# Performance work log

Measured on AMD Instinct MI355X. Metric: run time of the kernel, lower is better.

## Reference

```python
import jax, jax.numpy as jnp
import numpy as np

B, H, S, D = 4, 16, 2048, 64

def setup_inputs() -> dict:
    key = jax.random.key(0)
    kq, kk, kv = jax.random.split(key, 3)
    query = jax.random.normal(kq, (B, H, S, D), dtype=jnp.float32)
    key_t = jax.random.normal(kk, (B, H, S, D), dtype=jnp.float32)
    value = jax.random.normal(kv, (B, H, S, D), dtype=jnp.float32)
    return {"query": query, "key": key_t, "value": value}

def reference(query, key, value):
    d = query.shape[-1]
    scale = 1.0 / jnp.sqrt(jnp.asarray(d, dtype=query.dtype))
    # scores: [B, H, S_q, S_k]
    scores = jnp.einsum('bhqd,bhkd->bhqk', query, key) * scale
    p_attn = jax.nn.softmax(scores, axis=-1)
    # out: [B, H, S_q, D]
    return jnp.einsum('bhqk,bhkd->bhqd', p_attn, value)
```

## Files before the change

kernel.cpp:

```cpp
#include <hip/hip_runtime.h>
#include <hip/hip_bf16.h>


constexpr int Sdim = 2048;
constexpr int Ddim = 64;
constexpr int QBLK = 128;
constexpr int KVBLK = 64;
constexpr int NBH = 64;
constexpr int NT = Sdim / KVBLK;
constexpr int TILE_E = KVBLK * Ddim;
constexpr float QSCALE = 0.125f * 1.44269504f;
constexpr float DEFER_THR = 11.0f;

typedef __attribute__((ext_vector_type(8))) short short8;
typedef __attribute__((ext_vector_type(4))) float f32x4;
typedef __attribute__((ext_vector_type(4))) unsigned short ushort4v;
typedef __attribute__((ext_vector_type(2))) unsigned int uint2v;

typedef __attribute__((address_space(1))) const unsigned int GU32;
typedef __attribute__((address_space(3))) unsigned int LU32;

__device__ __forceinline__ unsigned short f2bf(float f) {
    union { float f; unsigned int u; } v; v.f = f;
    unsigned int r = v.u + 0x7FFFu + ((v.u >> 16) & 1u);
    return (unsigned short)(r >> 16);
}

__device__ __forceinline__ unsigned int cvt_pk_bf16(float lo, float hi) {
    unsigned int r;
    asm("v_cvt_pk_bf16_f32 %0, %1, %2" : "=v"(r) : "v"(lo), "v"(hi));
    return r;
}

__device__ __forceinline__ void gload_lds16(const unsigned short* g, unsigned short* l) {
    __builtin_amdgcn_global_load_lds((GU32*)g, (LU32*)l, 16, 0, 0);
}

__global__ __launch_bounds__(256)
void prep_k(const float* __restrict__ Kg, unsigned short* __restrict__ Kbf) {
    size_t idx = ((size_t)blockIdx.x * 256 + threadIdx.x) * 4;
    int c0 = (int)(idx & 63);
    size_t row = idx >> 6;
    int swz = ((int)row & 7) << 3;
    float4 f = *(const float4*)(Kg + idx);
    ushort4v h;
    h.x = f2bf(f.x); h.y = f2bf(f.y); h.z = f2bf(f.z); h.w = f2bf(f.w);
    *(ushort4v*)(Kbf + (row << 6) + (c0 ^ swz)) = h;
}

__global__ __launch_bounds__(256)
void prep_v(const float* __restrict__ Vg, unsigned short* __restrict__ Vtb) {
    __shared__ unsigned short Vl[KVBLK][Ddim + 4];
    int bh = blockIdx.x >> 5, t = blockIdx.x & 31;
    const float* src = Vg + ((size_t)bh * Sdim + t * KVBLK) * Ddim;
    unsigned short* dst = Vtb + ((size_t)bh * NT + t) * TILE_E;

    {
        int kv = threadIdx.x >> 2;
        int dq = (threadIdx.x & 3) * 16;
#pragma unroll
        for (int i = 0; i < 4; ++i) {
            float4 f = *(const float4*)(src + (size_t)kv * Ddim + dq + 4 * i);
            ushort4v h;
            h.x = f2bf(f.x); h.y = f2bf(f.y); h.z = f2bf(f.z); h.w = f2bf(f.w);
            *(ushort4v*)&Vl[kv][dq + 4 * i] = h;
        }
    }
    __syncthreads();
    {
        int d  = threadIdx.x >> 2;
        int sc = (threadIdx.x & 3) * 16;
        int swzd = (d & 7) << 3;
#pragma unroll
        for (int u = 0; u < 4; ++u) {
            int s0 = sc + 4 * u;
            int kc = s0 >> 5, g = (s0 >> 3) & 3, h = (s0 >> 2) & 1;
            int kvb = 32 * kc + 16 * h + 4 * g;
            ushort4v o;
            o.x = Vl[kvb + 0][d]; o.y = Vl[kvb + 1][d];
            o.z = Vl[kvb + 2][d]; o.w = Vl[kvb + 3][d];
            *(ushort4v*)(dst + (size_t)d * KVBLK + (s0 ^ swzd)) = o;
        }
    }
}

__global__ __launch_bounds__(512, 4)
void attn_fwd_fast(const float* __restrict__ Qg, const unsigned short* __restrict__ Kbf,
                   const unsigned short* __restrict__ Vtb, float* __restrict__ Og)
{
    __shared__ unsigned short Kt[2][KVBLK][Ddim];
    __shared__ unsigned short Vt[2][Ddim][KVBLK];

    const int tid = threadIdx.x;
    const int w   = tid >> 6;
    const int l   = tid & 63;
    const int g   = l >> 4;
    const int q   = l & 15;
    const int swz = (q & 7) << 3;

    const int bh = blockIdx.y;
    const size_t base = (size_t)bh * Sdim * Ddim;
    const int q0 = blockIdx.x * QBLK;

    const unsigned short* kbase = Kbf + base;
    const unsigned short* vbase = Vtb + base;
    const int eo = tid * 8;

    short8 qf[2];
    {
        const float* qrow = Qg + base + (size_t)(q0 + w * 16 + q) * Ddim;
#pragma unroll
        for (int kc = 0; kc < 2; ++kc) {
            float fv[8];
            *(float4*)(fv)     = *(const float4*)(qrow + kc * 32 + g * 8);
            *(float4*)(fv + 4) = *(const float4*)(qrow + kc * 32 + g * 8 + 4);
            short8 r;
#pragma unroll
            for (int j = 0; j < 8; ++j) r[j] = (short)f2bf(fv[j] * QSCALE);
            qf[kc] = r;
        }
    }

    f32x4 o[4];
#pragma unroll
    for (int dt = 0; dt < 4; ++dt)
#pragma unroll
        for (int r = 0; r < 4; ++r) o[dt][r] = 0.0f;
    float m_run = 0.0f;
    float l_part = 0.0f;

    union PU { unsigned int u[4]; short8 s8; };

    gload_lds16(kbase + eo, &Kt[0][0][0] + w * 512);
    gload_lds16(vbase + eo, &Vt[0][0][0] + w * 512);

    for (int t = 0; t < NT; ++t) {
        const int cur = t & 1;
        if (t + 1 < NT) {
            const unsigned short* kn = kbase + (size_t)(t + 1) * TILE_E;
            const unsigned short* vn = vbase + (size_t)(t + 1) * TILE_E;
            gload_lds16(kn + eo, &Kt[cur ^ 1][0][0] + w * 512);
            gload_lds16(vn + eo, &Vt[cur ^ 1][0][0] + w * 512);
            asm volatile("s_waitcnt vmcnt(2)" ::: "memory");
        } else {
            asm volatile("s_waitcnt vmcnt(0)" ::: "memory");
        }
        __builtin_amdgcn_s_barrier();
        __builtin_amdgcn_sched_barrier(0);

        f32x4 sa[4];
#pragma unroll
        for (int nt = 0; nt < 4; ++nt)
#pragma unroll
            for (int r = 0; r < 4; ++r) sa[nt][r] = -m_run;
        __builtin_amdgcn_s_setprio(1);
#pragma unroll
        for (int kc = 0; kc < 2; ++kc)
#pragma unroll
            for (int nt = 0; nt < 4; ++nt) {
                const short8 kf = *(const short8*)&Kt[cur][nt * 16 + q][(kc * 32 + g * 8) ^ swz];
                sa[nt] = __builtin_amdgcn_mfma_f32_16x16x32_bf16(kf, qf[kc], sa[nt], 0, 0, 0);
            }
        __builtin_amdgcn_s_setprio(0);

        f32x4 m4 = sa[0];
#pragma unroll
        for (int nt = 1; nt < 4; ++nt)
#pragma unroll
            for (int r = 0; r < 4; ++r) m4[r] = fmaxf(m4[r], sa[nt][r]);
        float mx = fmaxf(fmaxf(m4[0], m4[1]), fmaxf(m4[2], m4[3]));
        mx = fmaxf(mx, __shfl_xor(mx, 16));
        mx = fmaxf(mx, __shfl_xor(mx, 32));

        PU pa[2];
        float ts = 0.0f;
        if (__all(mx <= DEFER_THR)) {
#pragma unroll
            for (int nt = 0; nt < 4; ++nt) {
                float e0 = exp2f(sa[nt][0]), e1 = exp2f(sa[nt][1]);
                float e2 = exp2f(sa[nt][2]), e3 = exp2f(sa[nt][3]);
                ts += (e0 + e1) + (e2 + e3);
                pa[nt >> 1].u[(nt & 1) * 2 + 0] = cvt_pk_bf16(e0, e1);
                pa[nt >> 1].u[(nt & 1) * 2 + 1] = cvt_pk_bf16(e2, e3);
            }
            l_part += ts;
        } else {
            float fr = exp2f(-mx);
            m_run += mx;
#pragma unroll
            for (int nt = 0; nt < 4; ++nt) {
                float e0 = exp2f(sa[nt][0] - mx), e1 = exp2f(sa[nt][1] - mx);
                float e2 = exp2f(sa[nt][2] - mx), e3 = exp2f(sa[nt][3] - mx);
                ts += (e0 + e1) + (e2 + e3);
                pa[nt >> 1].u[(nt & 1) * 2 + 0] = cvt_pk_bf16(e0, e1);
                pa[nt >> 1].u[(nt & 1) * 2 + 1] = cvt_pk_bf16(e2, e3);
            }
            l_part = l_part * fr + ts;
            float frb[4];
#pragma unroll
            for (int r = 0; r < 4; ++r) frb[r] = __shfl(fr, 4 * g + r);
#pragma unroll
            for (int dt = 0; dt < 4; ++dt)
#pragma unroll
                for (int r = 0; r < 4; ++r) o[dt][r] *= frb[r];
        }

        __builtin_amdgcn_s_setprio(1);
#pragma unroll
        for (int kc = 0; kc < 2; ++kc)
#pragma unroll
            for (int dt = 0; dt < 4; ++dt) {
                const short8 vf = *(const short8*)&Vt[cur][dt * 16 + q][(kc * 32 + g * 8) ^ swz];
                o[dt] = __builtin_amdgcn_mfma_f32_16x16x32_bf16(pa[kc].s8, vf, o[dt], 0, 0, 0);
            }
        __builtin_amdgcn_s_setprio(0);

        if (t + 1 < NT) {
            __builtin_amdgcn_sched_barrier(0);
            __builtin_amdgcn_s_barrier();
        }
    }

    l_part += __shfl_xor(l_part, 16);
    l_part += __shfl_xor(l_part, 32);
    float inv = 1.0f / l_part;
    float invb[4];
#pragma unroll
    for (int r = 0; r < 4; ++r) invb[r] = __shfl(inv, 4 * g + r);
#pragma unroll
    for (int r = 0; r < 4; ++r) {
        float* orow = Og + base + (size_t)(q0 + w * 16 + 4 * g + r) * Ddim;
#pragma unroll
        for (int dt = 0; dt < 4; ++dt) orow[dt * 16 + q] = o[dt][r] * invb[r];
    }
}

__global__ __launch_bounds__(256, 4)
void attn_fwd_slow(const float* __restrict__ Qg, const float* __restrict__ Kg,
                   const float* __restrict__ Vg, float* __restrict__ Og)
{
    __shared__ unsigned short Kt[KVBLK][Ddim];
    __shared__ unsigned short Vt[Ddim][KVBLK];
    __shared__ unsigned short Pt[4][16][KVBLK];

    const int tid = threadIdx.x;
    const int w   = tid >> 6;
    const int l   = tid & 63;
    const int g   = l >> 4;
    const int q   = l & 15;
    const int swz = (q & 7) << 3;

    const size_t base = (size_t)blockIdx.y * Sdim * Ddim;
    const int q0 = blockIdx.x * 64;

    short8 qf[2];
    {
        const float* qrow = Qg + base + (size_t)(q0 + w * 16 + q) * Ddim;
#pragma unroll
        for (int kc = 0; kc < 2; ++kc) {
            float fv[8];
            *(float4*)(fv)     = *(const float4*)(qrow + kc * 32 + g * 8);
            *(float4*)(fv + 4) = *(const float4*)(qrow + kc * 32 + g * 8 + 4);
            short8 r;
#pragma unroll
            for (int j = 0; j < 8; ++j) r[j] = (short)f2bf(fv[j] * QSCALE);
            qf[kc] = r;
        }
    }

    f32x4 o[4];
#pragma unroll
    for (int dt = 0; dt < 4; ++dt)
#pragma unroll
        for (int r = 0; r < 4; ++r) o[dt][r] = 0.0f;
    float m_run = -INFINITY, l_run = 0.0f;

    for (int t = 0; t < NT; ++t) {
        __syncthreads();
        {
            const float* Ksrc = Kg + base + (size_t)t * KVBLK * Ddim;
            const float* Vsrc = Vg + base + (size_t)t * KVBLK * Ddim;
#pragma unroll
            for (int it = 0; it < 4; ++it) {
                int idx = it * 1024 + tid * 4;
                int r = idx >> 6, c = idx & 63;
                float4 kf4 = *(const float4*)(Ksrc + idx);
                ushort4v hk;
                hk.x = f2bf(kf4.x); hk.y = f2bf(kf4.y);
                hk.z = f2bf(kf4.z); hk.w = f2bf(kf4.w);
                *(ushort4v*)&Kt[r][c ^ ((r & 7) << 3)] = hk;
            }
            {
                const int d = l;
                const int vswz = (d & 7) << 3;
#pragma unroll
                for (int i = 0; i < 4; ++i) {
                    int kv0 = w * 16 + i * 4;
                    float a0 = Vsrc[(size_t)(kv0 + 0) * Ddim + d];
                    float a1 = Vsrc[(size_t)(kv0 + 1) * Ddim + d];
                    float a2 = Vsrc[(size_t)(kv0 + 2) * Ddim + d];
                    float a3 = Vsrc[(size_t)(kv0 + 3) * Ddim + d];
                    ushort4v hv;
                    hv.x = f2bf(a0); hv.y = f2bf(a1);
                    hv.z = f2bf(a2); hv.w = f2bf(a3);
                    *(ushort4v*)&Vt[d][kv0 ^ vswz] = hv;
                }
            }
        }
        __syncthreads();

        f32x4 sa[4];
#pragma unroll
        for (int nt = 0; nt < 4; ++nt)
#pragma unroll
            for (int r = 0; r < 4; ++r) sa[nt][r] = 0.0f;
#pragma unroll
        for (int kc = 0; kc < 2; ++kc)
#pragma unroll
            for (int nt = 0; nt < 4; ++nt) {
                const short8 kf = *(const short8*)&Kt[nt * 16 + q][(kc * 32 + g * 8) ^ swz];
                sa[nt] = __builtin_amdgcn_mfma_f32_16x16x32_bf16(kf, qf[kc], sa[nt], 0, 0, 0);
            }

        float mx = sa[0][0];
#pragma unroll
        for (int nt = 0; nt < 4; ++nt)
#pragma unroll
            for (int r = 0; r < 4; ++r) mx = fmaxf(mx, sa[nt][r]);
        mx = fmaxf(mx, __shfl_xor(mx, 16));
        mx = fmaxf(mx, __shfl_xor(mx, 32));
        float mnew = fmaxf(m_run, mx);
        float fr = exp2f(m_run - mnew);
        m_run = mnew;

        float p[4][4];
        float s = 0.0f;
#pragma unroll
        for (int nt = 0; nt < 4; ++nt)
#pragma unroll
            for (int r = 0; r < 4; ++r) {
                float e = exp2f(sa[nt][r] - mnew);
                p[nt][r] = e; s += e;
            }
        s += __shfl_xor(s, 16);
        s += __shfl_xor(s, 32);
        l_run = l_run * fr + s;

#pragma unroll
        for (int nt = 0; nt < 4; ++nt) {
            uint2v pp;
            pp.x = cvt_pk_bf16(p[nt][0], p[nt][1]);
            pp.y = cvt_pk_bf16(p[nt][2], p[nt][3]);
            *(uint2v*)&Pt[w][q][(nt * 16 + 4 * g) ^ swz] = pp;
        }

        float frb[4];
#pragma unroll
        for (int r = 0; r < 4; ++r) frb[r] = __shfl(fr, 4 * g + r);
#pragma unroll
        for (int dt = 0; dt < 4; ++dt)
#pragma unroll
            for (int r = 0; r < 4; ++r) o[dt][r] *= frb[r];

#pragma unroll
        for (int kc = 0; kc < 2; ++kc) {
            const short8 pf = *(const short8*)&Pt[w][q][(kc * 32 + g * 8) ^ swz];
#pragma unroll
            for (int dt = 0; dt < 4; ++dt) {
                const short8 vf = *(const short8*)&Vt[dt * 16 + q][(kc * 32 + g * 8) ^ swz];
                o[dt] = __builtin_amdgcn_mfma_f32_16x16x32_bf16(pf, vf, o[dt], 0, 0, 0);
            }
        }
    }

    float inv = 1.0f / l_run;
    float invb[4];
#pragma unroll
    for (int r = 0; r < 4; ++r) invb[r] = __shfl(inv, 4 * g + r);
#pragma unroll
    for (int r = 0; r < 4; ++r) {
        float* orow = Og + base + (size_t)(q0 + w * 16 + 4 * g + r) * Ddim;
#pragma unroll
        for (int dt = 0; dt < 4; ++dt) orow[dt * 16 + q] = o[dt][r] * invb[r];
    }
}

extern "C" void kernel_launch(void* const* d_in, const int* in_sizes, int n_in,
                              void* d_out, int out_size, void* d_ws, size_t ws_size,
                              hipStream_t stream) {
    const float* Q = (const float*)d_in[0];
    const float* K = (const float*)d_in[1];
    const float* V = (const float*)d_in[2];
    float* O = (float*)d_out;
    const size_t elems = (size_t)NBH * Sdim * Ddim;
    const size_t need  = elems * 2 * 2;
    if (ws_size >= need) {
        unsigned short* Kbf = (unsigned short*)d_ws;
        unsigned short* Vtb = Kbf + elems;
        prep_k<<<dim3((unsigned)(elems / 4 / 256)), dim3(256), 0, stream>>>(K, Kbf);
        prep_v<<<dim3(NBH * NT), dim3(256), 0, stream>>>(V, Vtb);
        attn_fwd_fast<<<dim3(Sdim / QBLK, NBH), dim3(512), 0, stream>>>(Q, Kbf, Vtb, O);
    } else {
        attn_fwd_slow<<<dim3(Sdim / 64, NBH), dim3(256), 0, stream>>>(Q, K, V, O);
    }
}
```

Measured before the change: 249.5 us.

## Give each wave two query sub-tiles to reuse K/V fragments; merge prep kernels

The attention kernel now runs 4 waves of 256 threads instead of 8, and each wave handles 32 query rows as two 16-row groups. Every K and V fragment read from LDS now feeds two MFMAs, which halves LDS read traffic per FLOP and doubles the loads each thread issues per tile. The K and V bf16 prep kernels are merged into a single launch to save one kernel launch. In exchange, register use per thread roughly doubles for accumulators and scores, and there are fewer waves per workgroup to hide latency.

New measurement: 424.4 us. +70.1%, slower.

```diff
diff --git a/kernel.cpp b/kernel.cpp
--- a/kernel.cpp
+++ b/kernel.cpp
@@ -15,6 +15,7 @@
 typedef __attribute__((ext_vector_type(8))) short short8;
 typedef __attribute__((ext_vector_type(4))) float f32x4;
 typedef __attribute__((ext_vector_type(4))) unsigned short ushort4v;
+typedef __attribute__((ext_vector_type(4))) unsigned int uint4v;
 typedef __attribute__((ext_vector_type(2))) unsigned int uint2v;
 
 typedef __attribute__((address_space(1))) const unsigned int GU32;
@@ -36,25 +37,28 @@
     __builtin_amdgcn_global_load_lds((GU32*)g, (LU32*)l, 16, 0, 0);
 }
 
+constexpr int KPB = (NBH * Sdim * Ddim) / 4 / 256;
+constexpr int VPB = NBH * NT;
+
 __global__ __launch_bounds__(256)
-void prep_k(const float* __restrict__ Kg, unsigned short* __restrict__ Kbf) {
-    size_t idx = ((size_t)blockIdx.x * 256 + threadIdx.x) * 4;
-    int c0 = (int)(idx & 63);
-    size_t row = idx >> 6;
-    int swz = ((int)row & 7) << 3;
-    float4 f = *(const float4*)(Kg + idx);
-    ushort4v h;
-    h.x = f2bf(f.x); h.y = f2bf(f.y); h.z = f2bf(f.z); h.w = f2bf(f.w);
-    *(ushort4v*)(Kbf + (row << 6) + (c0 ^ swz)) = h;
-}
-
-__global__ __launch_bounds__(256)
-void prep_v(const float* __restrict__ Vg, unsigned short* __restrict__ Vtb) {
+void prep_kv(const float* __restrict__ Kg, const float* __restrict__ Vg,
+             unsigned short* __restrict__ Kbf, unsigned short* __restrict__ Vtb) {
     __shared__ unsigned short Vl[KVBLK][Ddim + 4];
-    int bh = blockIdx.x >> 5, t = blockIdx.x & 31;
+    if (blockIdx.x < KPB) {
+        size_t idx = ((size_t)blockIdx.x * 256 + threadIdx.x) * 4;
+        int c0 = (int)(idx & 63);
+        size_t row = idx >> 6;
+        int swz = ((int)row & 7) << 3;
+        float4 f = *(const float4*)(Kg + idx);
+        ushort4v h;
+        h.x = f2bf(f.x); h.y = f2bf(f.y); h.z = f2bf(f.z); h.w = f2bf(f.w);
+        *(ushort4v*)(Kbf + (row << 6) + (c0 ^ swz)) = h;
+        return;
+    }
+    int bid = blockIdx.x - KPB;
+    int bh = bid >> 5, t = bid & 31;
     const float* src = Vg + ((size_t)bh * Sdim + t * KVBLK) * Ddim;
     unsigned short* dst = Vtb + ((size_t)bh * NT + t) * TILE_E;
-
     {
         int kv = threadIdx.x >> 2;
         int dq = (threadIdx.x & 3) * 16;
@@ -84,12 +88,12 @@
     }
 }
 
-__global__ __launch_bounds__(512, 4)
+__global__ __launch_bounds__(256, 4)
 void attn_fwd_fast(const float* __restrict__ Qg, const unsigned short* __restrict__ Kbf,
                    const unsigned short* __restrict__ Vtb, float* __restrict__ Og)
 {
-    __shared__ unsigned short Kt[2][KVBLK][Ddim];
-    __shared__ unsigned short Vt[2][Ddim][KVBLK];
+    __shared__ unsigned short Kt[2][TILE_E];
+    __shared__ unsigned short Vt[2][TILE_E];
 
     const int tid = threadIdx.x;
     const int w   = tid >> 6;
@@ -105,10 +109,12 @@
     const unsigned short* kbase = Kbf + base;
     const unsigned short* vbase = Vtb + base;
     const int eo = tid * 8;
-
-    short8 qf[2];
-    {
-        const float* qrow = Qg + base + (size_t)(q0 + w * 16 + q) * Ddim;
+    const int stoff = w * 512;
+
+    short8 qf[2][2];
+#pragma unroll
+    for (int gg = 0; gg < 2; ++gg) {
+        const float* qrow = Qg + base + (size_t)(q0 + w * 32 + gg * 16 + q) * Ddim;
 #pragma unroll
         for (int kc = 0; kc < 2; ++kc) {
             float fv[8];
@@ -117,102 +123,130 @@
             short8 r;
 #pragma unroll
             for (int j = 0; j < 8; ++j) r[j] = (short)f2bf(fv[j] * QSCALE);
-            qf[kc] = r;
-        }
-    }
-
-    f32x4 o[4];
-#pragma unroll
-    for (int dt = 0; dt < 4; ++dt)
-#pragma unroll
-        for (int r = 0; r < 4; ++r) o[dt][r] = 0.0f;
-    float m_run = 0.0f;
-    float l_part = 0.0f;
-
-    union PU { unsigned int u[4]; short8 s8; };
-
-    gload_lds16(kbase + eo, &Kt[0][0][0] + w * 512);
-    gload_lds16(vbase + eo, &Vt[0][0][0] + w * 512);
+            qf[gg][kc] = r;
+        }
+    }
+
+    f32x4 o_[2][4];
+#pragma unroll
+    for (int gg = 0; gg < 2; ++gg)
+#pragma unroll
+        for (int dt = 0; dt < 4; ++dt)
+#pragma unroll
+            for (int r = 0; r < 4; ++r) o_[gg][dt][r] = 0.0f;
+    float m_run[2] = {0.0f, 0.0f};
+    float l_part[2] = {0.0f, 0.0f};
+
+    gload_lds16(kbase + eo,        &Kt[0][0] + stoff);
+    gload_lds16(kbase + 2048 + eo, &Kt[0][0] + 2048 + stoff);
+    gload_lds16(vbase + eo,        &Vt[0][0] + stoff);
+    gload_lds16(vbase + 2048 + eo, &Vt[0][0] + 2048 + stoff);
 
     for (int t = 0; t < NT; ++t) {
         const int cur = t & 1;
         if (t + 1 < NT) {
-            const unsigned short* kn = kbase + (size_t)(t + 1) * TILE_E;
-            const unsigned short* vn = vbase + (size_t)(t + 1) * TILE_E;
-            gload_lds16(kn + eo, &Kt[cur ^ 1][0][0] + w * 512);
-            gload_lds16(vn + eo, &Vt[cur ^ 1][0][0] + w * 512);
-            asm volatile("s_waitcnt vmcnt(2)" ::: "memory");
+            const size_t toff = (size_t)(t + 1) * TILE_E + eo;
+            unsigned short* kd = &Kt[cur ^ 1][0];
+            unsigned short* vd = &Vt[cur ^ 1][0];
+            gload_lds16(kbase + toff,        kd + stoff);
+            gload_lds16(kbase + toff + 2048, kd + 2048 + stoff);
+            gload_lds16(vbase + toff,        vd + stoff);
+            gload_lds16(vbase + toff + 2048, vd + 2048 + stoff);
+            asm volatile("s_waitcnt vmcnt(4)" ::: "memory");
         } else {
             asm volatile("s_waitcnt vmcnt(0)" ::: "memory");
         }
         __builtin_amdgcn_s_barrier();
         __builtin_amdgcn_sched_barrier(0);
 
-        f32x4 sa[4];
-#pragma unroll
-        for (int nt = 0; nt < 4; ++nt)
-#pragma unroll
-            for (int r = 0; r < 4; ++r) sa[nt][r] = -m_run;
+        const unsigned short* kb = &Kt[cur][0];
+        const unsigned short* vb = &Vt[cur][0];
+
+        f32x4 sa[2][4];
+#pragma unroll
+        for (int gg = 0; gg < 2; ++gg)
+#pragma unroll
+            for (int nt = 0; nt < 4; ++nt)
+#pragma unroll
+                for (int r = 0; r < 4; ++r) sa[gg][nt][r] = -m_run[gg];
         __builtin_amdgcn_s_setprio(1);
 #pragma unroll
         for (int kc = 0; kc < 2; ++kc)
 #pragma unroll
             for (int nt = 0; nt < 4; ++nt) {
-                const short8 kf = *(const short8*)&Kt[cur][nt * 16 + q][(kc * 32 + g * 8) ^ swz];
-                sa[nt] = __builtin_amdgcn_mfma_f32_16x16x32_bf16(kf, qf[kc], sa[nt], 0, 0, 0);
+                const short8 kf = *(const short8*)(kb + (nt * 16 + q) * Ddim + ((kc * 32 + g * 8) ^ swz));
+                sa[0][nt] = __builtin_amdgcn_mfma_f32_16x16x32_bf16(kf, qf[0][kc], sa[0][nt], 0, 0, 0);
+                sa[1][nt] = __builtin_amdgcn_mfma_f32_16x16x32_bf16(kf, qf[1][kc], sa[1][nt], 0, 0, 0);
             }
         __builtin_amdgcn_s_setprio(0);
 
-        f32x4 m4 = sa[0];
-#pragma unroll
-        for (int nt = 1; nt < 4; ++nt)
-#pragma unroll
-            for (int r = 0; r < 4; ++r) m4[r] = fmaxf(m4[r], sa[nt][r]);
-        float mx = fmaxf(fmaxf(m4[0], m4[1]), fmaxf(m4[2], m4[3]));
-        mx = fmaxf(mx, __shfl_xor(mx, 16));
-        mx = fmaxf(mx, __shfl_xor(mx, 32));
-
-        PU pa[2];
-        float ts = 0.0f;
-        if (__all(mx <= DEFER_THR)) {
-#pragma unroll
-            for (int nt = 0; nt < 4; ++nt) {
-                float e0 = exp2f(sa[nt][0]), e1 = exp2f(sa[nt][1]);
-                float e2 = exp2f(sa[nt][2]), e3 = exp2f(sa[nt][3]);
-                ts += (e0 + e1) + (e2 + e3);
-                pa[nt >> 1].u[(nt & 1) * 2 + 0] = cvt_pk_bf16(e0, e1);
-                pa[nt >> 1].u[(nt & 1) * 2 + 1] = cvt_pk_bf16(e2, e3);
-            }
-            l_part += ts;
+        float mx[2];
+#pragma unroll
+        for (int gg = 0; gg < 2; ++gg) {
+            f32x4 m4 = sa[gg][0];
+#pragma unroll
+            for (int nt = 1; nt < 4; ++nt)
+#pragma unroll
+                for (int r = 0; r < 4; ++r) m4[r] = fmaxf(m4[r], sa[gg][nt][r]);
+            float m = fmaxf(fmaxf(m4[0], m4[1]), fmaxf(m4[2], m4[3]));
+            m = fmaxf(m, __shfl_xor(m, 16));
+            m = fmaxf(m, __shfl_xor(m, 32));
+            mx[gg] = m;
+        }
+
+        uint4v pav[2][2];
+        if (__all(fmaxf(mx[0], mx[1]) <= DEFER_THR)) {
+#pragma unroll
+            for (int gg = 0; gg < 2; ++gg) {
+                float ts = 0.0f;
+#pragma unroll
+                for (int nt = 0; nt < 4; ++nt) {
+                    float e0 = exp2f(sa[gg][nt][0]), e1 = exp2f(sa[gg][nt][1]);
+                    float e2 = exp2f(sa[gg][nt][2]), e3 = exp2f(sa[gg][nt][3]);
+                    ts += (e0 + e1) + (e2 + e3);
+                    pav[gg][nt >> 1][(nt & 1) * 2 + 0] = cvt_pk_bf16(e0, e1);
+                    pav[gg][nt >> 1][(nt & 1) * 2 + 1] = cvt_pk_bf16(e2, e3);
+                }
+                l_part[gg] += ts;
+            }
         } else {
-            float fr = exp2f(-mx);
-            m_run += mx;
-#pragma unroll
-            for (int nt = 0; nt < 4; ++nt) {
-                float e0 = exp2f(sa[nt][0] - mx), e1 = exp2f(sa[nt][1] - mx);
-                float e2 = exp2f(sa[nt][2] - mx), e3 = exp2f(sa[nt][3] - mx);
-                ts += (e0 + e1) + (e2 + e3);
-                pa[nt >> 1].u[(nt & 1) * 2 + 0] = cvt_pk_bf16(e0, e1);
-                pa[nt >> 1].u[(nt & 1) * 2 + 1] = cvt_pk_bf16(e2, e3);
-            }
-            l_part = l_part * fr + ts;
-            float frb[4];
-#pragma unroll
-            for (int r = 0; r < 4; ++r) frb[r] = __shfl(fr, 4 * g + r);
-#pragma unroll
-            for (int dt = 0; dt < 4; ++dt)
-#pragma unroll
-                for (int r = 0; r < 4; ++r) o[dt][r] *= frb[r];
+#pragma unroll
+            for (int gg = 0; gg < 2; ++gg) {
+                float m = mx[gg];
+                float fr = exp2f(-m);
+                m_run[gg] += m;
+                float ts = 0.0f;
+#pragma unroll
+                for (int nt = 0; nt < 4; ++nt) {
+                    float e0 = exp2f(sa[gg][nt][0] - m), e1 = exp2f(sa[gg][nt][1] - m);
+                    float e2 = exp2f(sa[gg][nt][2] - m), e3 = exp2f(sa[gg][nt][3] - m);
+                    ts += (e0 + e1) + (e2 + e3);
+                    pav[gg][nt >> 1][(nt & 1) * 2 + 0] = cvt_pk_bf16(e0, e1);
+                    pav[gg][nt >> 1][(nt & 1) * 2 + 1] = cvt_pk_bf16(e2, e3);
+                }
+                l_part[gg] = l_part[gg] * fr + ts;
+                float frb[4];
+#pragma unroll
+                for (int r = 0; r < 4; ++r) frb[r] = __shfl(fr, 4 * g + r);
+#pragma unroll
+                for (int dt = 0; dt < 4; ++dt)
+#pragma unroll
+                    for (int r = 0; r < 4; ++r) o_[gg][dt][r] *= frb[r];
+            }
         }
 
         __builtin_amdgcn_s_setprio(1);
 #pragma unroll
-        for (int kc = 0; kc < 2; ++kc)
+        for (int kc = 0; kc < 2; ++kc) {
+            const short8 pa0 = __builtin_bit_cast(short8, pav[0][kc]);
+            const short8 pa1 = __builtin_bit_cast(short8, pav[1][kc]);
 #pragma unroll
             for (int dt = 0; dt < 4; ++dt) {
-                const short8 vf = *(const short8*)&Vt[cur][dt * 16 + q][(kc * 32 + g * 8) ^ swz];
-                o[dt] = __builtin_amdgcn_mfma_f32_16x16x32_bf16(pa[kc].s8, vf, o[dt], 0, 0, 0);
-            }
+                const short8 vf = *(const short8*)(vb + (dt * 16 + q) * Ddim + ((kc * 32 + g * 8) ^ swz));
+                o_[0][dt] = __builtin_amdgcn_mfma_f32_16x16x32_bf16(pa0, vf, o_[0][dt], 0, 0, 0);
+                o_[1][dt] = __builtin_amdgcn_mfma_f32_16x16x32_bf16(pa1, vf, o_[1][dt], 0, 0, 0);
+            }
+        }
         __builtin_amdgcn_s_setprio(0);
 
         if (t + 1 < NT) {
@@ -221,17 +255,21 @@
         }
     }
 
-    l_part += __shfl_xor(l_part, 16);
-    l_part += __shfl_xor(l_part, 32);
-    float inv = 1.0f / l_part;
-    float invb[4];
-#pragma unroll
-    for (int r = 0; r < 4; ++r) invb[r] = __shfl(inv, 4 * g + r);
-#pragma unroll
-    for (int r = 0; r < 4; ++r) {
-        float* orow = Og + base + (size_t)(q0 + w * 16 + 4 * g + r) * Ddim;
-#pragma unroll
-        for (int dt = 0; dt < 4; ++dt) orow[dt * 16 + q] = o[dt][r] * invb[r];
+#pragma unroll
+    for (int gg = 0; gg < 2; ++gg) {
+        float lp = l_part[gg];
+        lp += __shfl_xor(lp, 16);
+        lp += __shfl_xor(lp, 32);
+        float inv = 1.0f / lp;
+        float invb[4];
+#pragma unroll
+        for (int r = 0; r < 4; ++r) invb[r] = __shfl(inv, 4 * g + r);
+#pragma unroll
+        for (int r = 0; r < 4; ++r) {
+            float* orow = Og + base + (size_t)(q0 + w * 32 + gg * 16 + 4 * g + r) * Ddim;
+#pragma unroll
+            for (int dt = 0; dt < 4; ++dt) orow[dt * 16 + q] = o_[gg][dt][r] * invb[r];
+        }
     }
 }
 
@@ -239,8 +277,8 @@
 void attn_fwd_slow(const float* __restrict__ Qg, const float* __restrict__ Kg,
                    const float* __restrict__ Vg, float* __restrict__ Og)
 {
-    __shared__ unsigned short Kt[KVBLK][Ddim];
-    __shared__ unsigned short Vt[Ddim][KVBLK];
+    __shared__ unsigned short Kts[KVBLK][Ddim];
+    __shared__ unsigned short Vts[Ddim][KVBLK];
     __shared__ unsigned short Pt[4][16][KVBLK];
 
     const int tid = threadIdx.x;
@@ -288,7 +326,7 @@
                 ushort4v hk;
                 hk.x = f2bf(kf4.x); hk.y = f2bf(kf4.y);
                 hk.z = f2bf(kf4.z); hk.w = f2bf(kf4.w);
-                *(ushort4v*)&Kt[r][c ^ ((r & 7) << 3)] = hk;
+                *(ushort4v*)&Kts[r][c ^ ((r & 7) << 3)] = hk;
             }
             {
                 const int d = l;
@@ -303,7 +341,7 @@
                     ushort4v hv;
                     hv.x = f2bf(a0); hv.y = f2bf(a1);
                     hv.z = f2bf(a2); hv.w = f2bf(a3);
-                    *(ushort4v*)&Vt[d][kv0 ^ vswz] = hv;
+                    *(ushort4v*)&Vts[d][kv0 ^ vswz] = hv;
                 }
             }
         }
@@ -318,7 +356,7 @@
         for (int kc = 0; kc < 2; ++kc)
 #pragma unroll
             for (int nt = 0; nt < 4; ++nt) {
-                const short8 kf = *(const short8*)&Kt[nt * 16 + q][(kc * 32 + g * 8) ^ swz];
+                const short8 kf = *(const short8*)&Kts[nt * 16 + q][(kc * 32 + g * 8) ^ swz];
                 sa[nt] = __builtin_amdgcn_mfma_f32_16x16x32_bf16(kf, qf[kc], sa[nt], 0, 0, 0);
             }
 
@@ -367,7 +405,7 @@
             const short8 pf = *(const short8*)&Pt[w][q][(kc * 32 + g * 8) ^ swz];
 #pragma unroll
             for (int dt = 0; dt < 4; ++dt) {
-                const short8 vf = *(const short8*)&Vt[dt * 16 + q][(kc * 32 + g * 8) ^ swz];
+                const short8 vf = *(const short8*)&Vts[dt * 16 + q][(kc * 32 + g * 8) ^ swz];
                 o[dt] = __builtin_amdgcn_mfma_f32_16x16x32_bf16(pf, vf, o[dt], 0, 0, 0);
             }
         }
@@ -397,9 +435,8 @@
     if (ws_size >= need) {
         unsigned short* Kbf = (unsigned short*)d_ws;
         unsigned short* Vtb = Kbf + elems;
-        prep_k<<<dim3((unsigned)(elems / 4 / 256)), dim3(256), 0, stream>>>(K, Kbf);
-        prep_v<<<dim3(NBH * NT), dim3(256), 0, stream>>>(V, Vtb);
-        attn_fwd_fast<<<dim3(Sdim / QBLK, NBH), dim3(512), 0, stream>>>(Q, Kbf, Vtb, O);
+        prep_kv<<<dim3(KPB + VPB), dim3(256), 0, stream>>>(K, V, Kbf, Vtb);
+        attn_fwd_fast<<<dim3(Sdim / QBLK, NBH), dim3(256), 0, stream>>>(Q, Kbf, Vtb, O);
     } else {
         attn_fwd_slow<<<dim3(Sdim / 64, NBH), dim3(256), 0, stream>>>(Q, K, V, O);
     }
```
